# Kernel tuning notes

Hardware: AMD Instinct MI355X
Metric: run time of the kernel (lower is better)

The kernel has to match this reference:

```python
import jax, jax.numpy as jnp
import numpy as np

K = 16
EPS = 1e-5
SLOPE = 0.01  # nn.LeakyReLU default


def _bn(x, g, b):
    # BatchNorm1d in training mode applied to [N, C, k] in torch == normalize
    # per-channel over (N, k) axes of [N, k, C] here. Biased variance (ddof=0).
    m = x.mean(axis=(0, 1))
    v = x.var(axis=(0, 1))
    return (x - m) * jax.lax.rsqrt(v + EPS) * g + b


def _lrelu(x):
    return jnp.where(x >= 0, x, SLOPE * x)


def setup_inputs() -> dict:
    key = jax.random.key(0)
    ks = jax.random.split(key, 24)
    N, CIN, COUT = 8192, 256, 256
    s = 0.05
    inp = {
        "fea_i": jax.random.normal(ks[0], (N, CIN), jnp.float32),
        "fea_last": jax.random.normal(ks[1], (N, CIN), jnp.float32),
        "xyz_i": jax.random.uniform(ks[2], (N, 3), jnp.float32),
        "xyz_last": jax.random.uniform(ks[3], (N, 3), jnp.float32),
        "t_i": jnp.float32(2.0),
        "t_last": jnp.float32(1.0),
        # lin_p: Linear(4,64) -> BN(64) -> LeakyReLU -> Linear(64,COUT)
        "wp1": jax.random.normal(ks[4], (4, 64), jnp.float32) * s,
        "bp1": jnp.zeros((64,), jnp.float32),
        "gp": jnp.ones((64,), jnp.float32),
        "bp": jnp.zeros((64,), jnp.float32),
        "wp2": jax.random.normal(ks[5], (64, COUT), jnp.float32) * s,
        "bp2": jnp.zeros((COUT,), jnp.float32),
        # lin_q / lin_k / lin_v
        "wq": jax.random.normal(ks[6], (CIN, COUT), jnp.float32) * s,
        "bq": jnp.zeros((COUT,), jnp.float32),
        "wk": jax.random.normal(ks[7], (CIN, COUT), jnp.float32) * s,
        "bk": jnp.zeros((COUT,), jnp.float32),
        "wv": jax.random.normal(ks[8], (CIN, COUT), jnp.float32) * s,
        "bv": jnp.zeros((COUT,), jnp.float32),
        # lin_w: BN -> LeakyReLU -> Linear(COUT,COUT) -> BN -> LeakyReLU
        "gw1": jnp.ones((COUT,), jnp.float32),
        "bw1": jnp.zeros((COUT,), jnp.float32),
        "ww": jax.random.normal(ks[9], (COUT, COUT), jnp.float32) * s,
        "bw": jnp.zeros((COUT,), jnp.float32),
        "gw2": jnp.ones((COUT,), jnp.float32),
        "bw2": jnp.zeros((COUT,), jnp.float32),
    }
    return inp


def reference(fea_i, fea_last, xyz_i, xyz_last, t_i, t_last,
              wp1, bp1, gp, bp, wp2, bp2,
              wq, bq, wk, bk, wv, bv,
              gw1, bw1, ww, bw, gw2, bw2):
    # k-NN: for each query point in xyz_last, K nearest points in xyz_i
    d2 = (jnp.sum(xyz_last * xyz_last, -1)[:, None]
          + jnp.sum(xyz_i * xyz_i, -1)[None, :]
          - 2.0 * xyz_last @ xyz_i.T)              # [N, N]
    idx = jax.lax.top_k(-d2, K)[1]                 # [N, K] neighbor idx into xyz_i

    fi = fea_i[idx]                                # [N, K, CIN]
    xi = xyz_i[idx]                                # [N, K, 3]
    # pe = xyzt_i - xyzt_last ; the gathered "last" side is the query point itself
    pe = jnp.concatenate([xi - xyz_last[:, None, :],
                          (t_i - t_last) * jnp.ones_like(xi[..., :1])], axis=-1)  # [N,K,4]
    pe = pe @ wp1 + bp1
    pe = _lrelu(_bn(pe, gp, bp))
    pe = pe @ wp2 + bp2                            # [N, K, COUT]

    q = fea_last @ wq + bq                         # [N, COUT], broadcast over K
    w = q[:, None, :] - (fi @ wk + bk) + pe        # [N, K, COUT]
    w = _lrelu(_bn(w, gw1, bw1))
    w = w @ ww + bw
    w = _lrelu(_bn(w, gw2, bw2))
    w = jax.nn.softmax(w, axis=1)                  # softmax over K neighbors

    v = fi @ wv + bv + pe                          # [N, K, COUT]
    return jnp.sum(w * v, axis=1)                  # [N, COUT]
```

## Files before the change

kernel.cpp:

```cpp
#include <hip/hip_runtime.h>
#include <hip/hip_bf16.h>
#include <math.h>

#define N     8192
#define KNN   16
#define NK    (N*KNN)
#define C     256
#define CH    64
#define EPS   1e-5f
#define SLOPE 0.01f
#define LISTMAX 512

typedef __hip_bfloat16 bf16;
typedef short bfrag __attribute__((ext_vector_type(8)));
typedef float ffrag __attribute__((ext_vector_type(4)));

__device__ __forceinline__ float b2f(bf16 x){ return __bfloat162float(x); }
__device__ __forceinline__ bf16  f2b(float x){ return __float2bfloat16(x); }
__device__ __forceinline__ float b2fu(unsigned short s){
    return __uint_as_float(((unsigned)s) << 16);
}
__device__ __forceinline__ unsigned short f2bu(float x){
    union { bf16 h; unsigned short s; } u; u.h = f2b(x); return u.s;
}

union BF8 { unsigned short s[8]; uint4 u; };

template<typename T> __device__ __forceinline__ float ldv(const void* p, int i);
template<> __device__ __forceinline__ float ldv<float>(const void* p, int i){
    return ((const float*)p)[i];
}
template<> __device__ __forceinline__ float ldv<bf16>(const void* p, int i){
    return __bfloat162float(((const bf16*)p)[i]);
}
__device__ __forceinline__ bool is_f32(const void* ti){
    return ((const unsigned short*)ti)[0] == 0;
}

template<typename T>
__device__ __forceinline__ void stage8(const void* src, size_t off,
                                       unsigned short* dst){
    if (sizeof(T) == 4){
        const float4* s = (const float4*)((const float*)src + off);
        float4 a = s[0], b = s[1];
        BF8 o;
        o.s[0]=f2bu(a.x); o.s[1]=f2bu(a.y); o.s[2]=f2bu(a.z); o.s[3]=f2bu(a.w);
        o.s[4]=f2bu(b.x); o.s[5]=f2bu(b.y); o.s[6]=f2bu(b.z); o.s[7]=f2bu(b.w);
        *(uint4*)dst = o.u;
    } else {
        *(uint4*)dst = *(const uint4*)((const unsigned short*)src + off);
    }
}

__device__ __forceinline__ int mbcnt64(unsigned long long b){
    return __builtin_amdgcn_mbcnt_hi((unsigned)(b>>32),
           __builtin_amdgcn_mbcnt_lo((unsigned)b, 0));
}
__device__ __forceinline__ unsigned d2key(float d2){
    unsigned u = __float_as_uint(d2);
    return u ^ (((unsigned)(((int)u) >> 31)) | 0x80000000u);
}

__device__ __align__(256) int    g_idx[NK];
__device__ __align__(256) float  g_S[4096];
__device__ __align__(256) float  g_Rep[4*64*256];
__device__ __align__(256) float  g_M2[2048*9];
__device__ __align__(256) float4 g_pts[N];
__device__ __align__(256) float4 g_qlast[N];
__device__ __align__(256) int    g_cellCnt[4096];
__device__ __align__(256) int    g_cellStart[4100];
__device__ __align__(256) int    g_cellCur[4096];
__device__ __align__(256) float4 g_spts[N];
__device__ __align__(256) int    g_sidx[N];
__device__ __align__(256) unsigned short g_qT [C*C];
__device__ __align__(256) unsigned short g_kT [C*C];
__device__ __align__(256) unsigned short g_vT [C*C];
__device__ __align__(256) unsigned short g_wwT[C*C];
__device__ __align__(256) unsigned short g_p2T[C*CH];
__device__ __align__(256) unsigned short g_q  [N*C];
__device__ __align__(256) unsigned short g_fkb[N*C];
__device__ __align__(256) unsigned short g_fvb[N*C];
__device__ __align__(256) bf16   g_w1[NK*C];
__device__ __align__(256) bf16   g_vv[NK*C];
__device__ __align__(256) bf16   g_w2[NK*C];

__device__ __forceinline__ int cell_of(float4 c){
    int cx = (int)(c.x*16.f); cx = cx<0?0:(cx>15?15:cx);
    int cy = (int)(c.y*16.f); cy = cy<0?0:(cy>15?15:cy);
    int cz = (int)(c.z*16.f); cz = cz<0?0:(cz>15?15:cz);
    return (cz<<8) | (cy<<4) | cx;
}

__global__ __launch_bounds__(256) void kprepall(const void* xyz_i,
        const void* xyz_last,
        const void* wq, const void* wk, const void* wv, const void* ww,
        const void* wp2, const void* ti_){
#pragma clang fp contract(off)
    const int b = blockIdx.x, tid = threadIdx.x;
    const bool f = is_f32(ti_);
    if (b < 64){
        int i = b*256 + tid;
        #pragma unroll
        for (int k = 0; k < 4; k++) g_Rep[i*4 + k] = 0.f;
        if (b < 16) g_S[i] = 0.f;
    } else if (b < 96){
        int p = (b-64)*256 + tid;
        float x = f ? ldv<float>(xyz_i, p*3+0) : ldv<bf16>(xyz_i, p*3+0);
        float y = f ? ldv<float>(xyz_i, p*3+1) : ldv<bf16>(xyz_i, p*3+1);
        float z = f ? ldv<float>(xyz_i, p*3+2) : ldv<bf16>(xyz_i, p*3+2);
        float4 c = make_float4(x, y, z, (x*x + y*y) + z*z);
        g_pts[p] = c;
        atomicAdd(&g_cellCnt[cell_of(c)], 1);
    } else if (b < 128){
        int p = (b-96)*256 + tid;
        float x = f ? ldv<float>(xyz_last, p*3+0) : ldv<bf16>(xyz_last, p*3+0);
        float y = f ? ldv<float>(xyz_last, p*3+1) : ldv<bf16>(xyz_last, p*3+1);
        float z = f ? ldv<float>(xyz_last, p*3+2) : ldv<bf16>(xyz_last, p*3+2);
        g_qlast[p] = make_float4(x, y, z, 0.f);
    } else {
        const void* src; unsigned short* dst; int K; int i0;
        if      (b <  384){ src=wq;  dst=g_qT;  K=256; i0=(b- 128)*256; }
        else if (b <  640){ src=wk;  dst=g_kT;  K=256; i0=(b- 384)*256; }
        else if (b <  896){ src=wv;  dst=g_vT;  K=256; i0=(b- 640)*256; }
        else if (b < 1152){ src=ww;  dst=g_wwT; K=256; i0=(b- 896)*256; }
        else              { src=wp2; dst=g_p2T; K=64;  i0=(b-1152)*256; }
        int i = i0 + tid;
        int k = i >> 8, n = i & 255;
        float v = f ? ldv<float>(src, i) : ldv<bf16>(src, i);
        dst[n*K + k] = f2bu(v);
    }
}

__global__ __launch_bounds__(256) void kscan(){
    __shared__ int sc[256];
    const int tid = threadIdx.x;
    int v[16]; int loc = 0;
    #pragma unroll
    for (int j = 0; j < 16; j++){
        v[j] = g_cellCnt[tid*16 + j];
        loc += v[j];
    }
    #pragma unroll
    for (int j = 0; j < 16; j++) g_cellCnt[tid*16 + j] = 0;
    sc[tid] = loc;
    __syncthreads();
    for (int s = 1; s < 256; s <<= 1){
        int t_ = (tid >= s) ? sc[tid - s] : 0;
        __syncthreads();
        sc[tid] += t_;
        __syncthreads();
    }
    int excl = sc[tid] - loc;
    #pragma unroll
    for (int j = 0; j < 16; j++){
        g_cellStart[tid*16 + j] = excl;
        g_cellCur[tid*16 + j]   = excl;
        excl += v[j];
    }
    if (tid == 255) g_cellStart[4096] = excl;
}
__global__ __launch_bounds__(256) void kscatter(){
    int p = blockIdx.x*256 + threadIdx.x;
    float4 c = g_pts[p];
    int pos = atomicAdd(&g_cellCur[cell_of(c)], 1);
    g_spts[pos] = c;
    g_sidx[pos] = p;
}

template<int D>
__device__ unsigned sel16(float qx, float qy, float qz, float sq, int lane){
#pragma clang fp contract(off)
    unsigned kk[D];
    #pragma unroll
    for (int i = 0; i < D; i++) kk[i] = 0xFFFFFFFFu;
    for (int t = 0; t < N/64; t++){
        float4 c = g_pts[t*64 + lane];
        float dot = (qx*c.x + qy*c.y) + qz*c.z;
        float d2  = (sq + c.w) - 2.0f*dot;
        unsigned u = d2key(d2);
        #pragma unroll
        for (int j = D-1; j > 0; --j){
            unsigned hi = (kk[j-1] > u) ? kk[j-1] : u;
            kk[j] = (kk[j] < hi) ? kk[j] : hi;
        }
        kk[0] = (kk[0] < u) ? kk[0] : u;
    }
    unsigned v16 = 0;
    for (int it = 0; it < 16; ++it){
        unsigned m = kk[0];
        #pragma unroll
        for (int s = 1; s < 64; s <<= 1){
            unsigned o = (unsigned)__shfl_xor((int)m, s, 64);
            m = (m < o) ? m : o;
        }
        unsigned long long ball = __ballot(kk[0] == m);
        int w = __ffsll(ball) - 1;
        if (lane == w){
            #pragma unroll
            for (int j = 0; j < D-1; j++) kk[j] = kk[j+1];
            kk[D-1] = 0xFFFFFFFFu;
        }
        v16 = m;
    }
    return v16;
}

__device__ int2 scan16(float qx, float qy, float qz, float sq, unsigned v16,
                       int lane, int* sure, int* tie){
#pragma clang fp contract(off)
    int nsure = 0, ntie = 0;
    for (int t = 0; t < N/64; t++){
        const int p = t*64 + lane;
        float4 c = g_pts[p];
        float dot = (qx*c.x + qy*c.y) + qz*c.z;
        float d2  = (sq + c.w) - 2.0f*dot;
        unsigned u = d2key(d2);
        bool bs = (u < v16), bt = (u == v16);
        unsigned long long Bs = __ballot(bs);
        unsigned long long Bt = __ballot(bt);
        if (bs){
            int pos = nsure + mbcnt64(Bs);
            if (pos < 16) sure[pos] = p;
        }
        if (bt){
            int pos = ntie + mbcnt64(Bt);
            if (pos < 16) tie[pos] = p;
        }
        nsure += (int)__popcll(Bs);
        ntie  += (int)__popcll(Bt);
    }
    return make_int2(nsure, ntie);
}

template<typename T>
__device__ void kknn_body(int bid, const void* xyz_last, int* sureL, int* tieL,
                          int* listL, float* momL){
#pragma clang fp contract(off)
    const int lane  = threadIdx.x & 63;
    const int wslot = threadIdx.x >> 6;
    const int q     = (bid*256 + threadIdx.x) >> 6;
    const float qx = ldv<T>(xyz_last, q*3+0);
    const float qy = ldv<T>(xyz_last, q*3+1);
    const float qz = ldv<T>(xyz_last, q*3+2);
    const float sq = (qx*qx + qy*qy) + qz*qz;
    int* sure = &sureL[wslot*16];
    int* tie  = &tieL [wslot*16];
    int* list = &listL[wslot*LISTMAX];

    int cqx = (int)(qx*16.f); cqx = cqx<0?0:(cqx>15?15:cqx);
    int cqy = (int)(qy*16.f); cqy = cqy<0?0:(cqy>15?15:cqy);
    int cqz = (int)(qz*16.f); cqz = cqz<0?0:(cqz>15?15:cqz);

    int cnt0 = 0, cnt1 = 0, cs0 = 0, cs1 = 0;
    #pragma unroll
    for (int h = 0; h < 2; h++){
        int idx = lane*2 + h;
        if (idx < 125){
            int iz = idx/25, r = idx - iz*25, iy = r/5, ix = r - iy*5;
            int cx = cqx+ix-2, cy = cqy+iy-2, cz = cqz+iz-2;
            if ((unsigned)cx < 16u && (unsigned)cy < 16u && (unsigned)cz < 16u){
                int cell = (cz<<8) | (cy<<4) | cx;
                int s = g_cellStart[cell], e = g_cellStart[cell+1];
                if (h == 0){ cs0 = s; cnt0 = e - s; }
                else       { cs1 = s; cnt1 = e - s; }
            }
        }
    }
    int tot = cnt0 + cnt1;
    int incl = tot;
    #pragma unroll
    for (int s = 1; s < 64; s <<= 1){
        int u = __shfl_up(incl, s, 64);
        if (lane >= s) incl += u;
    }
    const int Tn = __shfl(incl, 63, 64);
    int base = incl - tot;
    bool full = (Tn > LISTMAX) || (Tn < 16);
    unsigned v16 = 0;
    int nsure = 0, ntie = 0;
    if (!full){
        for (int i = 0; i < cnt0; i++) list[base+i] = cs0 + i;
        for (int i = 0; i < cnt1; i++) list[base+cnt0+i] = cs1 + i;
        unsigned kk[4] = {~0u,~0u,~0u,~0u};
        int chunks = (Tn + 63) >> 6;
        for (int t = 0; t < chunks; t++){
            int li = t*64 + lane;
            unsigned u = 0xFFFFFFFFu;
            if (li < Tn){
                float4 c = g_spts[list[li]];
                float dot = (qx*c.x + qy*c.y) + qz*c.z;
                u = d2key((sq + c.w) - 2.0f*dot);
            }
            #pragma unroll
            for (int j = 3; j > 0; --j){
                unsigned hi = (kk[j-1] > u) ? kk[j-1] : u;
                kk[j] = (kk[j] < hi) ? kk[j] : hi;
            }
            kk[0] = (kk[0] < u) ? kk[0] : u;
        }
        for (int it = 0; it < 16; ++it){
            unsigned m = kk[0];
            #pragma unroll
            for (int s = 1; s < 64; s <<= 1){
                unsigned o = (unsigned)__shfl_xor((int)m, s, 64);
                m = (m < o) ? m : o;
            }
            unsigned long long ball = __ballot(kk[0] == m);
            int w = __ffsll(ball) - 1;
            if (lane == w){
                kk[0]=kk[1]; kk[1]=kk[2]; kk[2]=kk[3]; kk[3]=0xFFFFFFFFu;
            }
            v16 = m;
        }
        const float h_ = 0.0625f;
        float dmin = 1e30f;
        if (cqx-2 > 0)  dmin = fminf(dmin, qx - (float)(cqx-2)*h_);
        if (cqx+3 < 16) dmin = fminf(dmin, (float)(cqx+3)*h_ - qx);
        if (cqy-2 > 0)  dmin = fminf(dmin, qy - (float)(cqy-2)*h_);
        if (cqy+3 < 16) dmin = fminf(dmin, (float)(cqy+3)*h_ - qy);
        if (cqz-2 > 0)  dmin = fminf(dmin, qz - (float)(cqz-2)*h_);
        if (cqz+3 < 16) dmin = fminf(dmin, (float)(cqz+3)*h_ - qz);
        unsigned ub = d2key(dmin*dmin);
        if (!(v16 < ub)) full = true;
    }
    if (!full){
        int chunks = (Tn + 63) >> 6;
        for (int t = 0; t < chunks; t++){
            int li = t*64 + lane;
            unsigned u = 0xFFFFFFFFu; int oi = 0;
            if (li < Tn){
                int pos = list[li];
                float4 c = g_spts[pos];
                oi = g_sidx[pos];
                float dot = (qx*c.x + qy*c.y) + qz*c.z;
                u = d2key((sq + c.w) - 2.0f*dot);
            }
            bool bs = (li < Tn) && (u < v16);
            bool bt = (li < Tn) && (u == v16);
            unsigned long long Bs = __ballot(bs);
            unsigned long long Bt = __ballot(bt);
            if (bs){
                int pos2 = nsure + mbcnt64(Bs);
                if (pos2 < 16) sure[pos2] = oi;
            }
            if (bt){
                int pos2 = ntie + mbcnt64(Bt);
                if (pos2 < 16) tie[pos2] = oi;
            }
            nsure += (int)__popcll(Bs);
            ntie  += (int)__popcll(Bt);
        }
        if (nsure > 16 || (ntie > 16 && nsure < 16)) full = true;
    }
    const bool gridok = !full;
    if (full){
        v16 = sel16<16>(qx, qy, qz, sq, lane);
        int2 c2 = scan16(qx, qy, qz, sq, v16, lane, sure, tie);
        nsure = c2.x; ntie = c2.y;
    }
    if (nsure > 16) nsure = 16;
    int vsel = 0;
    if (lane < 16 && lane < nsure) vsel = sure[lane];
    if (gridok){
        int tv = (lane < (ntie < 16 ? ntie : 16)) ? tie[lane] : 0x7FFFFFFF;
        #pragma unroll
        for (int k = 2; k <= 16; k <<= 1)
            #pragma unroll
            for (int j = k>>1; j > 0; j >>= 1){
                int o = __shfl_xor(tv, j, 64);
                bool asc = ((lane & k) == 0);
                bool low = ((lane & j) == 0);
                int mn = tv < o ? tv : o;
                int mx = tv < o ? o : tv;
                tv = (asc == low) ? mn : mx;
            }
        int tfrom = __shfl(tv, (lane - nsure) & 63, 64);
        if (lane < 16 && lane >= nsure) vsel = tfrom;
    } else {
        if (lane < 16 && lane >= nsure) vsel = tie[lane - nsure];
    }
    float dx = 0.f, dy = 0.f, dz = 0.f;
    if (lane < 16){
        if ((unsigned)vsel >= (unsigned)N) vsel = 0;
        g_idx[q*KNN + lane] = vsel;
        float4 c = g_pts[vsel];
        dx = c.x - qx; dy = c.y - qy; dz = c.z - qz;
    }
    float mm[9] = {dx, dy, dz, dx*dx, dx*dy, dx*dz, dy*dy, dy*dz, dz*dz};
    #pragma unroll
    for (int j = 0; j < 9; j++){
        #pragma unroll
        for (int s = 1; s < 16; s <<= 1)
            mm[j] += __shfl_xor(mm[j], s, 64);
    }
    if (lane == 0){
        #pragma unroll
        for (int j = 0; j < 9; j++) momL[wslot*9 + j] = mm[j];
    }
    __syncthreads();
    if (threadIdx.x < 9){
        int t = threadIdx.x;
        g_M2[bid*9 + t] = momL[t] + momL[9+t] + momL[18+t] + momL[27+t];
    }
}

template<typename T>
__device__ void kgemm3m_body(const void* A, const unsigned short* BT,
                             const void* bias, unsigned short* out,
                             unsigned short* Al, unsigned short* Bl,
                             int c0, int r0){
    const int tid  = threadIdx.x;
    const int lane = tid & 63, wv = tid >> 6;
    const int m    = lane & 15, qd = lane >> 4;
    const int rw   = (wv >> 1)*64, cw = (wv & 1)*64;
    ffrag acc[4][4];
    #pragma unroll
    for (int i = 0; i < 4; i++)
        #pragma unroll
        for (int j = 0; j < 4; j++)
            #pragma unroll
            for (int r = 0; r < 4; r++) acc[i][j][r] = 0.f;
    const int arow = tid >> 2, ach = tid & 3;
    for (int kt = 0; kt < 8; ++kt){
        __syncthreads();
        #pragma unroll
        for (int p = 0; p < 2; ++p){
            int row = arow + p*64;
            stage8<T>(A, (size_t)(r0+row)*C + kt*32 + ach*8, &Al[row*40 + ach*8]);
            *(uint4*)&Bl[row*40 + ach*8] =
                *(const uint4*)&BT[(c0+row)*C + kt*32 + ach*8];
        }
        __syncthreads();
        bfrag af[4], bfr[4];
        #pragma unroll
        for (int i = 0; i < 4; i++)
            af[i] = *(const bfrag*)&Al[(rw + i*16 + m)*40 + qd*8];
        #pragma unroll
        for (int j = 0; j < 4; j++)
            bfr[j] = *(const bfrag*)&Bl[(cw + j*16 + m)*40 + qd*8];
        #pragma unroll
        for (int i = 0; i < 4; i++)
            #pragma unroll
            for (int j = 0; j < 4; j++)
                acc[i][j] = __builtin_amdgcn_mfma_f32_16x16x32_bf16(
                                af[i], bfr[j], acc[i][j], 0, 0, 0);
    }
    float b4[4];
    #pragma unroll
    for (int j = 0; j < 4; j++) b4[j] = ldv<T>(bias, c0 + cw + j*16 + m);
    #pragma unroll
    for (int i = 0; i < 4; i++){
        #pragma unroll
        for (int r = 0; r < 4; r++){
            int row = r0 + rw + i*16 + qd*4 + r;
            unsigned short* orow = &out[(size_t)row*C];
            #pragma unroll
            for (int j = 0; j < 4; j++)
                orow[c0 + cw + j*16 + m] = f2bu(acc[i][j][r] + b4[j]);
        }
    }
}

template<typename T>
__device__ void kknngemm_body(int b, const void* xyz_last,
        const void* fea_i, const void* fea_last,
        const void* bq, const void* bk, const void* bv,
        unsigned char* smem){
    if (b < 384){
        unsigned short* Al = (unsigned short*)smem;
        unsigned short* Bl = Al + 128*40;
        const int which = b >> 7, rem = b & 127;
        const int c0 = (rem & 1)*128, r0 = (rem >> 1)*128;
        const void* A = (which==0) ? fea_last : fea_i;
        const unsigned short* BT = (which==0) ? g_qT : (which==1) ? g_kT : g_vT;
        const void* bias = (which==0) ? bq : (which==1) ? bk : bv;
        unsigned short* out = (which==0) ? g_q : (which==1) ? g_fkb : g_fvb;
        kgemm3m_body<T>(A, BT, bias, out, Al, Bl, c0, r0);
    } else {
        int* base   = (int*)smem;
        int* sureL  = base;
        int* tieL   = base + 64;
        int* listL  = base + 128;
        float* momL = (float*)(base + 128 + 4*LISTMAX);
        kknn_body<T>(b - 384, xyz_last, sureL, tieL, listL, momL);
    }
}
__global__ __launch_bounds__(256) void kknngemm(const void* xyz_last,
        const void* fea_i, const void* fea_last,
        const void* bq, const void* bk, const void* bv, const void* ti_){
    __shared__ __align__(16) unsigned char smem[20480];
    const int b = blockIdx.x;
    if (is_f32(ti_))
        kknngemm_body<float>(b, xyz_last, fea_i, fea_last, bq, bk, bv, smem);
    else
        kknngemm_body<bf16 >(b, xyz_last, fea_i, fea_last, bq, bk, bv, smem);
}

template<typename T>
__device__ void kfinpe_body(const void* wp1, const void* bp1,
                            const void* gp, const void* bp_,
                            const void* t_i, const void* t_last,
                            float* mTot, float* wred){
    const int tid = threadIdx.x, lane = tid & 63, wv = tid >> 6;
    float p[9];
    #pragma unroll
    for (int j = 0; j < 9; j++) p[j] = 0.f;
    for (int i = tid; i < 2048; i += 256){
        const float* m = &g_M2[i*9];
        #pragma unroll
        for (int j = 0; j < 9; j++) p[j] += m[j];
    }
    #pragma unroll
    for (int j = 0; j < 9; j++){
        #pragma unroll
        for (int s = 1; s < 64; s <<= 1) p[j] += __shfl_xor(p[j], s, 64);
    }
    if (lane == 0){
        #pragma unroll
        for (int j = 0; j < 9; j++) wred[wv*9 + j] = p[j];
    }
    __syncthreads();
    if (tid < 9) mTot[tid] = wred[tid] + wred[9+tid] + wred[18+tid] + wred[27+tid];
    __syncthreads();
    if (tid >= 64) return;
    const int c = tid;
    float M[9];
    #pragma unroll
    for (int j = 0; j < 9; j++) M[j] = mTot[j];
    const float w0 = ldv<T>(wp1, c),     w1 = ldv<T>(wp1, 64+c);
    const float w2 = ldv<T>(wp1, 128+c), w3 = ldv<T>(wp1, 192+c);
    const float dt = ldv<T>(t_i, 0) - ldv<T>(t_last, 0);
    const float be = dt*w3 + ldv<T>(bp1, c);
    const float NKf = (float)NK;
    float lin  = w0*M[0] + w1*M[1] + w2*M[2];
    float quad = w0*w0*M[3] + w1*w1*M[6] + w2*w2*M[8]
               + 2.f*(w0*w1*M[4] + w0*w2*M[5] + w1*w2*M[7]);
    float mean = (lin + NKf*be) / NKf;
    float ev2  = (quad + 2.f*be*lin + NKf*be*be) / NKf;
    float var  = ev2 - mean*mean;
    float sc   = ldv<T>(gp, c) * rsqrtf(var + EPS);
    g_S[128+c] = sc;
    g_S[192+c] = ldv<T>(bp_, c) - mean*sc;
}
__global__ void kfinpe(const void* wp1, const void* bp1, const void* gp,
                       const void* bp_, const void* t_i, const void* t_last){
    __shared__ float mTot[9];
    __shared__ float wred[4*9];
    if (is_f32(t_i)) kfinpe_body<float>(wp1, bp1, gp, bp_, t_i, t_last, mTot, wred);
    else             kfinpe_body<bf16 >(wp1, bp1, gp, bp_, t_i, t_last, mTot, wred);
}

__global__ void kfinalize(int Cn, int outOff, const void* g, const void* b,
                          const void* ti_, int repA){
    int c = threadIdx.x;
    if (c >= Cn) return;
    float s = 0.f, ss = 0.f;
    for (int r = 0; r < 64; r++){
        s  += g_Rep[((repA  )*64 + r)*256 + c];
        ss += g_Rep[((repA+1)*64 + r)*256 + c];
    }
    bool f = is_f32(ti_);
    float mean = s / (float)NK;
    float var  = ss / (float)NK - mean*mean;
    float gv = f ? ldv<float>(g, c) : ldv<bf16>(g, c);
    float bv = f ? ldv<float>(b, c) : ldv<bf16>(b, c);
    float sc = gv * rsqrtf(var + EPS);
    g_S[outOff+c]    = sc;
    g_S[outOff+Cn+c] = bv - mean*sc;
}

#define PE_LDP 68
template<typename T>
__device__ void kpe2m_body(const void* wp1, const void* bp1, const void* bp2,
                           const void* t_i, const void* t_last,
                           unsigned short* Apel, unsigned short* Bpl,
                           float* peL, int* gl, float* s1w, float* s2w){
    const int tid  = threadIdx.x;
    const int lane = tid & 63, wv = tid >> 6;
    const int m    = lane & 15, qd = lane >> 4;
    const int rw   = (wv >> 1)*64, cw = (wv & 1)*64;
    const int c0   = blockIdx.x*128, r0 = blockIdx.y*128;
    if (tid < 128) gl[tid] = g_idx[r0 + tid];
    { int row = tid >> 1, half = tid & 1;
      #pragma unroll
      for (int e = 0; e < 4; e++)
          *(uint4*)&Bpl[row*72 + half*32 + e*8] =
              *(const uint4*)&g_p2T[(c0+row)*CH + half*32 + e*8];
    }
    __syncthreads();
    { const int kp = lane;
      const float w0 = ldv<T>(wp1, kp),     w1 = ldv<T>(wp1, 64+kp);
      const float w2 = ldv<T>(wp1, 128+kp), w3 = ldv<T>(wp1, 192+kp);
      const float b0 = ldv<T>(bp1, kp);
      const float sc = g_S[128+kp], sh = g_S[128+64+kp];
      const float dt = ldv<T>(t_i, 0) - ldv<T>(t_last, 0);
      #pragma unroll 4
      for (int p = 0; p < 32; p++){
          int row = wv*32 + p;
          int R = r0 + row; int n = R >> 4; int g = gl[row];
          float4 cp = g_pts[g];
          float4 qp = g_qlast[n];
          float dx = cp.x - qp.x;
          float dy = cp.y - qp.y;
          float dz = cp.z - qp.z;
          float v = dx*w0 + dy*w1 + dz*w2 + dt*w3 + b0;
          v = v*sc + sh;
          v = (v >= 0.f) ? v : SLOPE*v;
          Apel[row*72 + kp] = f2bu(v);
      } }
    __syncthreads();
    ffrag acc[4][4];
    #pragma unroll
    for (int i = 0; i < 4; i++)
        #pragma unroll
        for (int j = 0; j < 4; j++)
            #pragma unroll
            for (int r = 0; r < 4; r++) acc[i][j][r] = 0.f;
    #pragma unroll
    for (int ks = 0; ks < 2; ++ks){
        bfrag af[4], bfr[4];
        #pragma unroll
        for (int i = 0; i < 4; i++)
            af[i] = *(const bfrag*)&Apel[(rw + i*16 + m)*72 + ks*32 + qd*8];
        #pragma unroll
        for (int j = 0; j < 4; j++)
            bfr[j] = *(const bfrag*)&Bpl[(cw + j*16 + m)*72 + ks*32 + qd*8];
        #pragma unroll
        for (int i = 0; i < 4; i++)
            #pragma unroll
            for (int j = 0; j < 4; j++)
                acc[i][j] = __builtin_amdgcn_mfma_f32_16x16x32_bf16(
                                af[i], bfr[j], acc[i][j], 0, 0, 0);
    }
    float bp2v[4];
    #pragma unroll
    for (int j = 0; j < 4; j++) bp2v[j] = ldv<T>(bp2, c0 + cw + j*16 + m);
    #pragma unroll
    for (int i = 0; i < 4; i++)
        #pragma unroll
        for (int j = 0; j < 4; j++)
            #pragma unroll
            for (int r = 0; r < 4; r++) acc[i][j][r] += bp2v[j];

    const int rep = blockIdx.y & 63;
    const int cg  = tid & 7;
    const int rg  = tid >> 3;
    for (int h = 0; h < 2; ++h){
        __syncthreads();
        if ((wv & 1) == h){
            #pragma unroll
            for (int i = 0; i < 4; i++)
                #pragma unroll
                for (int j = 0; j < 4; j++)
                    #pragma unroll
                    for (int r = 0; r < 4; r++)
                        peL[(rw + i*16 + qd*4 + r)*PE_LDP + j*16 + m]
                            = acc[i][j][r];
        }
        __syncthreads();
        float cs8[8], cq8[8];
        #pragma unroll
        for (int e = 0; e < 8; e++){ cs8[e] = 0.f; cq8[e] = 0.f; }
        #pragma unroll
        for (int rr = 0; rr < 4; rr++){
            int row = rg*4 + rr;
            int R = r0 + row; int n = R >> 4; int g = gl[row];
            int colb = c0 + h*64 + cg*8;
            BF8 qb, kb, vb;
            qb.u = *(const uint4*)&g_q  [(size_t)n*C + colb];
            kb.u = *(const uint4*)&g_fkb[(size_t)g*C + colb];
            vb.u = *(const uint4*)&g_fvb[(size_t)g*C + colb];
            float4 p0 = *(const float4*)&peL[row*PE_LDP + cg*8];
            float4 p1 = *(const float4*)&peL[row*PE_LDP + cg*8 + 4];
            float pe8[8] = {p0.x,p0.y,p0.z,p0.w,p1.x,p1.y,p1.z,p1.w};
            BF8 w1o, vvo;
            #pragma unroll
            for (int e = 0; e < 8; e++){
                float pv = pe8[e];
                unsigned short bb = f2bu(b2fu(qb.s[e]) - b2fu(kb.s[e]) + pv);
                w1o.s[e] = bb;
                float rv = b2fu(bb);
                cs8[e] += rv; cq8[e] += rv*rv;
                vvo.s[e] = f2bu(b2fu(vb.s[e]) + pv);
            }
            *(uint4*)&((unsigned short*)g_w1)[(size_t)R*C + colb] = w1o.u;
            *(uint4*)&((unsigned short*)g_vv)[(size_t)R*C + colb] = vvo.u;
        }
        #pragma unroll
        for (int e = 0; e < 8; e++){
            #pragma unroll
            for (int s_ = 8; s_ < 64; s_ <<= 1){
                cs8[e] += __shfl_xor(cs8[e], s_, 64);
                cq8[e] += __shfl_xor(cq8[e], s_, 64);
            }
        }
        if (lane < 8){
            #pragma unroll
            for (int e = 0; e < 8; e++){
                s1w[wv*64 + lane*8 + e] = cs8[e];
                s2w[wv*64 + lane*8 + e] = cq8[e];
            }
        }
        __syncthreads();
        if (tid < 64){
            float a = s1w[tid] + s1w[64+tid] + s1w[128+tid] + s1w[192+tid];
            float b = s2w[tid] + s2w[64+tid] + s2w[128+tid] + s2w[192+tid];
            atomicAdd(&g_Rep[(0*64 + rep)*256 + c0 + h*64 + tid], a);
            atomicAdd(&g_Rep[(1*64 + rep)*256 + c0 + h*64 + tid], b);
        }
    }
}
__global__ __launch_bounds__(256) void kpe2m(const void* wp1, const void* bp1,
        const void* bp2, const void* t_i, const void* t_last){
    __shared__ __align__(16) unsigned char smem[128*72*2*2];
    __shared__ int gl[128];
    __shared__ float s1w[256], s2w[256];
    unsigned short* Apel = (unsigned short*)smem;
    unsigned short* Bpl  = Apel + 128*72;
    float* peL = (float*)smem;
    if (is_f32(t_i))
        kpe2m_body<float>(wp1, bp1, bp2, t_i, t_last, Apel, Bpl, peL,
                          gl, s1w, s2w);
    else
        kpe2m_body<bf16 >(wp1, bp1, bp2, t_i, t_last, Apel, Bpl, peL,
                          gl, s1w, s2w);
}

template<typename T>
__device__ void kgemmww_body(const void* bw, unsigned short* Al,
                             unsigned short* Bl, float* scl, float* shl,
                             float* t1w, float* t2w){
    const int tid  = threadIdx.x;
    const int c0   = blockIdx.x*128, r0 = blockIdx.y*128;
    const int lane = tid & 63, wv = tid >> 6;
    const int m    = lane & 15, qd = lane >> 4;
    const int rw   = (wv >> 1)*64, cw = (wv & 1)*64;
    scl[tid] = g_S[768 + tid]; shl[tid] = g_S[768 + C + tid];
    ffrag acc[4][4];
    #pragma unroll
    for (int i = 0; i < 4; i++)
        #pragma unroll
        for (int j = 0; j < 4; j++)
            #pragma unroll
            for (int r = 0; r < 4; r++) acc[i][j][r] = 0.f;
    const int arow = tid >> 2, ach = tid & 3;
    for (int kt = 0; kt < 8; ++kt){
        __syncthreads();
        #pragma unroll
        for (int p = 0; p < 2; ++p){
            int row = arow + p*64;
            int kk  = kt*32 + ach*8;
            BF8 in, o;
            in.u = *(const uint4*)&g_w1[(size_t)(r0+row)*C + kk];
            #pragma unroll
            for (int e = 0; e < 8; e++){
                float x = b2fu(in.s[e]);
                x = x*scl[kk+e] + shl[kk+e];
                x = (x >= 0.f) ? x : SLOPE*x;
                o.s[e] = f2bu(x);
            }
            *(uint4*)&Al[row*40 + ach*8] = o.u;
            *(uint4*)&Bl[row*40 + ach*8] =
                *(const uint4*)&g_wwT[(c0+row)*C + kt*32 + ach*8];
        }
        __syncthreads();
        bfrag af[4], bf_[4];
        #pragma unroll
        for (int i = 0; i < 4; i++)
            af[i] = *(const bfrag*)&Al[(rw + i*16 + m)*40 + qd*8];
        #pragma unroll
        for (int j = 0; j < 4; j++)
            bf_[j] = *(const bfrag*)&Bl[(cw + j*16 + m)*40 + qd*8];
        #pragma unroll
        for (int i = 0; i < 4; i++)
            #pragma unroll
            for (int j = 0; j < 4; j++)
                acc[i][j] = __builtin_amdgcn_mfma_f32_16x16x32_bf16(
                                af[i], bf_[j], acc[i][j], 0, 0, 0);
    }
    float bwv[4];
    #pragma unroll
    for (int j = 0; j < 4; j++) bwv[j] = ldv<T>(bw, c0 + cw + j*16 + m);
    float cs[4] = {0.f,0.f,0.f,0.f}, cq[4] = {0.f,0.f,0.f,0.f};
    #pragma unroll
    for (int j = 0; j < 4; j++){
        int col = c0 + cw + j*16 + m;
        #pragma unroll
        for (int i = 0; i < 4; i++){
            #pragma unroll
            for (int r = 0; r < 4; r++){
                int row = r0 + rw + i*16 + qd*4 + r;
                unsigned short bb = f2bu(acc[i][j][r] + bwv[j]);
                ((unsigned short*)g_w2)[(size_t)row*C + col] = bb;
                float rv = b2fu(bb);
                cs[j] += rv; cq[j] += rv*rv;
            }
        }
    }
    #pragma unroll
    for (int j = 0; j < 4; j++){
        cs[j] += __shfl_xor(cs[j], 16, 64); cs[j] += __shfl_xor(cs[j], 32, 64);
        cq[j] += __shfl_xor(cq[j], 16, 64); cq[j] += __shfl_xor(cq[j], 32, 64);
    }
    if (lane < 16){
        #pragma unroll
        for (int j = 0; j < 4; j++){
            t1w[(wv>>1)*128 + cw + j*16 + lane] = cs[j];
            t2w[(wv>>1)*128 + cw + j*16 + lane] = cq[j];
        }
    }
    __syncthreads();
    if (tid < 128){
        float a = t1w[tid] + t1w[128+tid];
        float b = t2w[tid] + t2w[128+tid];
        int rep = blockIdx.y & 63;
        atomicAdd(&g_Rep[(2*64 + rep)*256 + c0 + tid], a);
        atomicAdd(&g_Rep[(3*64 + rep)*256 + c0 + tid], b);
    }
}
__global__ __launch_bounds__(256) void kgemmww(const void* bw, const void* ti_){
    __shared__ unsigned short Al[128*40];
    __shared__ unsigned short Bl[128*40];
    __shared__ float scl[C], shl[C];
    __shared__ float t1w[256], t2w[256];
    if (is_f32(ti_)) kgemmww_body<float>(bw, Al, Bl, scl, shl, t1w, t2w);
    else             kgemmww_body<bf16 >(bw, Al, Bl, scl, shl, t1w, t2w);
}

__global__ __launch_bounds__(256) void kfinal(void* out, const void* ti_){
    __shared__ unsigned short w2L[16*264];
    __shared__ unsigned short vvL[16*264];
    const int n = blockIdx.x, tid = threadIdx.x;
    const unsigned short* w2g = (const unsigned short*)g_w2 + (size_t)n*KNN*C;
    const unsigned short* vvg = (const unsigned short*)g_vv + (size_t)n*KNN*C;
    #pragma unroll
    for (int p = 0; p < 2; p++){
        int off = p*2048 + tid*8;
        int row = off >> 8, col = off & 255;
        *(uint4*)&w2L[row*264 + col] = *(const uint4*)&w2g[off];
        *(uint4*)&vvL[row*264 + col] = *(const uint4*)&vvg[off];
    }
    __syncthreads();
    const int c = tid;
    const float sc = g_S[1792+c], sh = g_S[1792+C+c];
    float u[KNN];
    float m = -3.4e38f;
    #pragma unroll
    for (int k = 0; k < KNN; k++){
        float x = b2fu(w2L[k*264 + c])*sc + sh;
        x = (x >= 0.f) ? x : SLOPE*x;
        u[k] = x; m = fmaxf(m, x);
    }
    float ssum = 0.f, o = 0.f;
    #pragma unroll
    for (int k = 0; k < KNN; k++){
        float e = __expf(u[k] - m);
        ssum += e;
        o += e * b2fu(vvL[k*264 + c]);
    }
    float r = o / ssum;
    if (is_f32(ti_)) ((float*)out)[(size_t)n*C + c] = r;
    else             ((bf16*)out)[(size_t)n*C + c] = f2b(r);
}

extern "C" void kernel_launch(void* const* d_in, const int* in_sizes, int n_in,
                              void* d_out, int out_size, void* d_ws, size_t ws_size,
                              hipStream_t stream){
    const void* fea_i    = d_in[0];
    const void* fea_last = d_in[1];
    const void* xyz_i    = d_in[2];
    const void* xyz_last = d_in[3];
    const void* t_i      = d_in[4];
    const void* t_last   = d_in[5];
    const void* wp1 = d_in[6];
    const void* bp1 = d_in[7];
    const void* gp  = d_in[8];
    const void* bp_ = d_in[9];
    const void* wp2 = d_in[10];
    const void* bp2 = d_in[11];
    const void* wq  = d_in[12];
    const void* bq  = d_in[13];
    const void* wk  = d_in[14];
    const void* bk  = d_in[15];
    const void* wv  = d_in[16];
    const void* bv  = d_in[17];
    const void* gw1 = d_in[18];
    const void* bw1 = d_in[19];
    const void* ww  = d_in[20];
    const void* bw  = d_in[21];
    const void* gw2 = d_in[22];
    const void* bw2 = d_in[23];

    kprepall<<<1216, 256, 0, stream>>>(xyz_i, xyz_last, wq, wk, wv, ww, wp2, t_i);
    kscan<<<1, 256, 0, stream>>>();
    kscatter<<<32, 256, 0, stream>>>();
    kknngemm<<<2432, 256, 0, stream>>>(xyz_last, fea_i, fea_last, bq, bk, bv, t_i);
    kfinpe<<<1, 256, 0, stream>>>(wp1, bp1, gp, bp_, t_i, t_last);
    kpe2m<<<dim3(2, NK/128), 256, 0, stream>>>(wp1, bp1, bp2, t_i, t_last);
    kfinalize<<<1, 256, 0, stream>>>(256, 768, gw1, bw1, t_i, 0);
    kgemmww<<<dim3(2, NK/128), 256, 0, stream>>>(bw, t_i);
    kfinalize<<<1, 256, 0, stream>>>(256, 1792, gw2, bw2, t_i, 2);
    kfinal<<<N, 256, 0, stream>>>(d_out, t_i);
}
```

Before: 302.9 us.

## Reorder query rows by spatial cell to improve gather locality

Query points are bucketed into the 16^3 spatial grid with a second count/scan/scatter pass, which yields a permutation g_qperm. kpe2m processes query rows in that permuted order, so each block's 8 queries are spatially close and their neighbor gathers of fea/key/value rows overlap more in cache. kfinal maps blocks back through the permutation when writing output. This adds a second scan pass, extra atomics and an indirection in the later kernels.

```diff
diff --git a/kernel.cpp b/kernel.cpp
--- a/kernel.cpp
+++ b/kernel.cpp
@@ -70,6 +70,10 @@
 __device__ __align__(256) int    g_cellCnt[4096];
 __device__ __align__(256) int    g_cellStart[4100];
 __device__ __align__(256) int    g_cellCur[4096];
+__device__ __align__(256) int    g_qcellCnt[4096];
+__device__ __align__(256) int    g_qcellStart[4100];
+__device__ __align__(256) int    g_qcellCur[4096];
+__device__ __align__(256) int    g_qperm[N];
 __device__ __align__(256) float4 g_spts[N];
 __device__ __align__(256) int    g_sidx[N];
 __device__ __align__(256) unsigned short g_qT [C*C];
@@ -116,7 +120,9 @@
         float x = f ? ldv<float>(xyz_last, p*3+0) : ldv<bf16>(xyz_last, p*3+0);
         float y = f ? ldv<float>(xyz_last, p*3+1) : ldv<bf16>(xyz_last, p*3+1);
         float z = f ? ldv<float>(xyz_last, p*3+2) : ldv<bf16>(xyz_last, p*3+2);
-        g_qlast[p] = make_float4(x, y, z, 0.f);
+        float4 c = make_float4(x, y, z, 0.f);
+        g_qlast[p] = c;
+        atomicAdd(&g_qcellCnt[cell_of(c)], 1);
     } else {
         const void* src; unsigned short* dst; int K; int i0;
         if      (b <  384){ src=wq;  dst=g_qT;  K=256; i0=(b- 128)*256; }
@@ -134,37 +140,52 @@
 __global__ __launch_bounds__(256) void kscan(){
     __shared__ int sc[256];
     const int tid = threadIdx.x;
-    int v[16]; int loc = 0;
-    #pragma unroll
-    for (int j = 0; j < 16; j++){
-        v[j] = g_cellCnt[tid*16 + j];
-        loc += v[j];
-    }
-    #pragma unroll
-    for (int j = 0; j < 16; j++) g_cellCnt[tid*16 + j] = 0;
-    sc[tid] = loc;
-    __syncthreads();
-    for (int s = 1; s < 256; s <<= 1){
-        int t_ = (tid >= s) ? sc[tid - s] : 0;
+    for (int pass = 0; pass < 2; ++pass){
+        int* cnt   = pass ? g_qcellCnt   : g_cellCnt;
+        int* start = pass ? g_qcellStart : g_cellStart;
+        int* cur   = pass ? g_qcellCur   : g_cellCur;
+        int v[16]; int loc = 0;
+        #pragma unroll
+        for (int j = 0; j < 16; j++){
+            v[j] = cnt[tid*16 + j];
+            loc += v[j];
+        }
+        #pragma unroll
+        for (int j = 0; j < 16; j++) cnt[tid*16 + j] = 0;
         __syncthreads();
-        sc[tid] += t_;
+        sc[tid] = loc;
         __syncthreads();
-    }
-    int excl = sc[tid] - loc;
-    #pragma unroll
-    for (int j = 0; j < 16; j++){
-        g_cellStart[tid*16 + j] = excl;
-        g_cellCur[tid*16 + j]   = excl;
-        excl += v[j];
-    }
-    if (tid == 255) g_cellStart[4096] = excl;
+        for (int s = 1; s < 256; s <<= 1){
+            int t_ = (tid >= s) ? sc[tid - s] : 0;
+            __syncthreads();
+            sc[tid] += t_;
+            __syncthreads();
+        }
+        int excl = sc[tid] - loc;
+        #pragma unroll
+        for (int j = 0; j < 16; j++){
+            start[tid*16 + j] = excl;
+            cur[tid*16 + j]   = excl;
+            excl += v[j];
+        }
+        if (tid == 255) start[4096] = excl;
+        __syncthreads();
+    }
 }
 __global__ __launch_bounds__(256) void kscatter(){
-    int p = blockIdx.x*256 + threadIdx.x;
-    float4 c = g_pts[p];
-    int pos = atomicAdd(&g_cellCur[cell_of(c)], 1);
-    g_spts[pos] = c;
-    g_sidx[pos] = p;
+    int b = blockIdx.x;
+    if (b < 32){
+        int p = b*256 + threadIdx.x;
+        float4 c = g_pts[p];
+        int pos = atomicAdd(&g_cellCur[cell_of(c)], 1);
+        g_spts[pos] = c;
+        g_sidx[pos] = p;
+    } else {
+        int p = (b-32)*256 + threadIdx.x;
+        float4 c = g_qlast[p];
+        int pos = atomicAdd(&g_qcellCur[cell_of(c)], 1);
+        g_qperm[pos] = p;
+    }
 }
 
 template<int D>
@@ -574,13 +595,18 @@
 __device__ void kpe2m_body(const void* wp1, const void* bp1, const void* bp2,
                            const void* t_i, const void* t_last,
                            unsigned short* Apel, unsigned short* Bpl,
-                           float* peL, int* gl, float* s1w, float* s2w){
+                           float* peL, int* gl, int* ql,
+                           float* s1w, float* s2w){
     const int tid  = threadIdx.x;
     const int lane = tid & 63, wv = tid >> 6;
     const int m    = lane & 15, qd = lane >> 4;
     const int rw   = (wv >> 1)*64, cw = (wv & 1)*64;
     const int c0   = blockIdx.x*128, r0 = blockIdx.y*128;
-    if (tid < 128) gl[tid] = g_idx[r0 + tid];
+    if (tid < 8) ql[tid] = g_qperm[blockIdx.y*8 + tid];
+    if (tid < 128){
+        int q = g_qperm[blockIdx.y*8 + (tid >> 4)];
+        gl[tid] = g_idx[q*KNN + (tid & 15)];
+    }
     { int row = tid >> 1, half = tid & 1;
       #pragma unroll
       for (int e = 0; e < 4; e++)
@@ -597,7 +623,7 @@
       #pragma unroll 4
       for (int p = 0; p < 32; p++){
           int row = wv*32 + p;
-          int R = r0 + row; int n = R >> 4; int g = gl[row];
+          int n = ql[row >> 4]; int g = gl[row];
           float4 cp = g_pts[g];
           float4 qp = g_qlast[n];
           float dx = cp.x - qp.x;
@@ -664,7 +690,7 @@
         #pragma unroll
         for (int rr = 0; rr < 4; rr++){
             int row = rg*4 + rr;
-            int R = r0 + row; int n = R >> 4; int g = gl[row];
+            int R = r0 + row; int n = ql[row >> 4]; int g = gl[row];
             int colb = c0 + h*64 + cg*8;
             BF8 qb, kb, vb;
             qb.u = *(const uint4*)&g_q  [(size_t)n*C + colb];
@@ -714,16 +740,17 @@
         const void* bp2, const void* t_i, const void* t_last){
     __shared__ __align__(16) unsigned char smem[128*72*2*2];
     __shared__ int gl[128];
+    __shared__ int ql[8];
     __shared__ float s1w[256], s2w[256];
     unsigned short* Apel = (unsigned short*)smem;
     unsigned short* Bpl  = Apel + 128*72;
     float* peL = (float*)smem;
     if (is_f32(t_i))
         kpe2m_body<float>(wp1, bp1, bp2, t_i, t_last, Apel, Bpl, peL,
-                          gl, s1w, s2w);
+                          gl, ql, s1w, s2w);
     else
         kpe2m_body<bf16 >(wp1, bp1, bp2, t_i, t_last, Apel, Bpl, peL,
-                          gl, s1w, s2w);
+                          gl, ql, s1w, s2w);
 }
 
 template<typename T>
@@ -830,9 +857,10 @@
 __global__ __launch_bounds__(256) void kfinal(void* out, const void* ti_){
     __shared__ unsigned short w2L[16*264];
     __shared__ unsigned short vvL[16*264];
-    const int n = blockIdx.x, tid = threadIdx.x;
-    const unsigned short* w2g = (const unsigned short*)g_w2 + (size_t)n*KNN*C;
-    const unsigned short* vvg = (const unsigned short*)g_vv + (size_t)n*KNN*C;
+    const int b = blockIdx.x, tid = threadIdx.x;
+    const int n = g_qperm[b];
+    const unsigned short* w2g = (const unsigned short*)g_w2 + (size_t)b*KNN*C;
+    const unsigned short* vvg = (const unsigned short*)g_vv + (size_t)b*KNN*C;
     #pragma unroll
     for (int p = 0; p < 2; p++){
         int off = p*2048 + tid*8;
@@ -893,7 +921,7 @@
 
     kprepall<<<1216, 256, 0, stream>>>(xyz_i, xyz_last, wq, wk, wv, ww, wp2, t_i);
     kscan<<<1, 256, 0, stream>>>();
-    kscatter<<<32, 256, 0, stream>>>();
+    kscatter<<<64, 256, 0, stream>>>();
     kknngemm<<<2432, 256, 0, stream>>>(xyz_last, fea_i, fea_last, bq, bk, bv, t_i);
     kfinpe<<<1, 256, 0, stream>>>(wp1, bp1, gp, bp_, t_i, t_last);
     kpe2m<<<dim3(2, NK/128), 256, 0, stream>>>(wp1, bp1, bp2, t_i, t_last);
```

Result: no change. 304.2 us (+0.4%).
